# Kernel tuning notes

Measured on AMD Instinct MI355X. Metric: run time of the kernel, lower is better.

The kernel has to match this reference:

```python
import jax, jax.numpy as jnp
import numpy as np

N = 50000      # total nodes
C = 128        # in_channels
G = 4          # num_groups
B = 50         # number of graphs
NPG = N // B   # nodes per graph = 1000
E = 250000     # total edges (intra-graph)
COUT = 128     # conv out_channels


def setup_inputs() -> dict:
    key = jax.random.key(0)
    ks = jax.random.split(key, 6)
    sc = 1.0 / np.sqrt(C)
    x = jax.random.normal(ks[0], (N, C), dtype=jnp.float32)
    W_group = jax.random.normal(ks[1], (C, G), dtype=jnp.float32) * sc
    W_self = jax.random.normal(ks[2], (C, COUT), dtype=jnp.float32) * sc
    W_nbr = jax.random.normal(ks[3], (C, COUT), dtype=jnp.float32) * sc
    b = jnp.zeros((COUT,), dtype=jnp.float32)
    # intra-graph edges: E//B edges per graph, endpoints offset by graph id
    epg = E // B
    offs = (jnp.arange(E, dtype=jnp.int32) // epg) * NPG
    src = offs + jax.random.randint(ks[4], (E,), 0, NPG, dtype=jnp.int32)
    dst = offs + jax.random.randint(ks[5], (E,), 0, NPG, dtype=jnp.int32)
    edge_index = jnp.stack([src, dst])
    batch = (jnp.arange(N, dtype=jnp.int32) // NPG)
    # expanded node e = i*G*NPG + g*NPG + j maps back to original node i*NPG + j
    eidx = jnp.arange(G * N, dtype=jnp.int32)
    group_ptr = (eidx // (G * NPG)) * NPG + (eidx % NPG)
    return dict(x=x, W_group=W_group, W_self=W_self, W_nbr=W_nbr, b=b,
                edge_index=edge_index, batch=batch, group_ptr=group_ptr)


def reference(x, W_group, W_self, W_nbr, b, edge_index, batch, group_ptr):
    # soft group assignment: s = softmax(x @ W_group).T -> [G, N]
    s = jax.nn.softmax(x @ W_group, axis=-1).T
    # outer-product expansion: [G, N, C]
    ex = s[:, :, None] * x[None, :, :]
    # per-graph cat ordering: (g, graph i, local j) -> i*G*NPG + g*NPG + j
    ex = ex.reshape(G, B, NPG, C).transpose(1, 0, 2, 3).reshape(G * N, C)
    # expanded adjacency: replicate each graph's edges once per group
    src, dst = edge_index[0], edge_index[1]
    goff = jnp.arange(G, dtype=src.dtype)[:, None] * NPG            # [G, 1]
    src_exp = ((src // NPG) * (G * NPG))[None, :] + goff + (src % NPG)[None, :]
    dst_exp = ((dst // NPG) * (G * NPG))[None, :] + goff + (dst % NPG)[None, :]
    src_exp = src_exp.reshape(-1)
    dst_exp = dst_exp.reshape(-1)
    # GraphConv on expanded graph: self transform + sum-aggregated neighbor transform
    msg = (ex @ W_nbr)[src_exp]                                      # [G*E, COUT]
    agg = jax.ops.segment_sum(msg, dst_exp, num_segments=G * N)
    out = ex @ W_self + agg + b                                      # [G*N, COUT]
    # scatter-reduce G group copies back onto N original nodes
    return jax.ops.segment_sum(out, group_ptr, num_segments=N)
```

## Files before the change

### kernel.cpp

```cpp
#include <hip/hip_runtime.h>

constexpr int N_NODES  = 50000;
constexpr int C_IN     = 128;
constexpr int C_OUT    = 128;
constexpr int E_EDGES  = 250000;
constexpr int G_GRP    = 4;
constexpr int TM       = 32;
constexpr int CAP      = 32;
constexpr int NXCD     = 8;


typedef __attribute__((ext_vector_type(8))) short     short8;
typedef __attribute__((ext_vector_type(4))) float     f32x4;
typedef __attribute__((ext_vector_type(2))) unsigned  u32x2;

__device__ __forceinline__ unsigned short f2bf(float f) {
    unsigned u = __builtin_bit_cast(unsigned, f);
    u += 0x7fffu + ((u >> 16) & 1u);
    return (unsigned short)(u >> 16);
}
__device__ __forceinline__ unsigned pack2(float lo, float hi) {
    return (unsigned)f2bf(lo) | ((unsigned)f2bf(hi) << 16);
}

__device__ __forceinline__ int xcd_swizzle(int bid, int nblocks) {
    int q = nblocks / NXCD, r = nblocks % NXCD;
    int xcd = bid % NXCD, lid = bid / NXCD;
    return (xcd < r ? xcd * (q + 1) : r * (q + 1) + (xcd - r) * q) + lid;
}

constexpr int ZERO_BLOCKS  = (N_NODES / 4 + 255) / 256;
constexpr int WPREP_BLOCKS = (C_OUT * 256) / 256;

__global__ __launch_bounds__(256) void zero_prep_kernel(
    int* __restrict__ cnt,
    const float* __restrict__ Wself, const float* __restrict__ Wnbr,
    unsigned short* __restrict__ WT)
{
    int b = blockIdx.x;
    if (b < ZERO_BLOCKS) {
        int idx = b * 256 + threadIdx.x;
        if (idx < N_NODES / 4)
            reinterpret_cast<int4*>(cnt)[idx] = make_int4(0, 0, 0, 0);
    } else {
        int idx = (b - ZERO_BLOCKS) * 256 + threadIdx.x;
        int c = idx >> 8, k = idx & 255;
        float v = (k < 128) ? Wself[k * C_OUT + c] : Wnbr[(k - 128) * C_OUT + c];
        WT[idx] = f2bf(v);
    }
}

constexpr int EDGE_BLOCKS = (E_EDGES + 255) / 256;

__global__ __launch_bounds__(256) void fill_kernel(
    const int* __restrict__ src, const int* __restrict__ dst,
    int* __restrict__ cnt, int* __restrict__ buckets)
{
    int e = blockIdx.x * 256 + threadIdx.x;
    if (e < E_EDGES) {
        int d = dst[e];
        int pos = atomicAdd(&cnt[d], 1);
        if (pos < CAP) buckets[(size_t)d * CAP + pos] = src[e];
    }
}

constexpr int GATHER_BLOCKS = N_NODES / 8;

__global__ __launch_bounds__(256) void gather_kernel(
    const float* __restrict__ x,
    const int* __restrict__ cnt,
    const int* __restrict__ buckets,
    unsigned short* __restrict__ xa_bf)
{
    int wg   = xcd_swizzle(blockIdx.x, GATHER_BLOCKS);
    int tid  = threadIdx.x;
    int n    = wg * 8 + (tid >> 5);
    int q    = tid & 31;

    const float4* x4 = reinterpret_cast<const float4*>(x);
    int d = cnt[n];
    if (d > CAP) d = CAP;
    const int* sp = buckets + (size_t)n * CAP;

    float ax = 0.f, ay = 0.f, az = 0.f, aw = 0.f;
    int e = 0;
    for (; e + 4 <= d; e += 4) {
        int s0 = sp[e], s1 = sp[e + 1], s2 = sp[e + 2], s3 = sp[e + 3];
        float4 v0 = x4[(size_t)s0 * 32 + q];
        float4 v1 = x4[(size_t)s1 * 32 + q];
        float4 v2 = x4[(size_t)s2 * 32 + q];
        float4 v3 = x4[(size_t)s3 * 32 + q];
        ax += (v0.x + v1.x) + (v2.x + v3.x);
        ay += (v0.y + v1.y) + (v2.y + v3.y);
        az += (v0.z + v1.z) + (v2.z + v3.z);
        aw += (v0.w + v1.w) + (v2.w + v3.w);
    }
    for (; e < d; ++e) {
        int s = sp[e];
        float4 v = x4[(size_t)s * 32 + q];
        ax += v.x; ay += v.y; az += v.z; aw += v.w;
    }

    u32x2 pk{pack2(ax, ay), pack2(az, aw)};
    *reinterpret_cast<u32x2*>(&xa_bf[(size_t)n * 128 + q * 4]) = pk;
}

constexpr int GEMM_BLOCKS = (N_NODES + TM - 1) / TM;

__global__ __launch_bounds__(256) void mfma_gemm_kernel(
    const float* __restrict__ x,
    const unsigned short* __restrict__ xa_bf,
    const unsigned short* __restrict__ WT,
    const float* __restrict__ bias,
    float* __restrict__ out)
{
    __shared__ unsigned char Ab[TM * 512];

    int wg = xcd_swizzle(blockIdx.x, GEMM_BLOCKS);
    const int tid  = threadIdx.x;
    const int row0 = wg * TM;

    #pragma unroll
    for (int i = 0; i < 4; ++i) {
        int idx = tid + i * 256;
        int r = idx >> 5, q = idx & 31;
        int n = row0 + r;
        float4 v = make_float4(0.f, 0.f, 0.f, 0.f);
        if (n < N_NODES) v = reinterpret_cast<const float4*>(x)[(size_t)n * 32 + q];
        unsigned lo = pack2(v.x, v.y), hi = pack2(v.z, v.w);
        int byte = (r * 512 + q * 8) ^ ((r & 7) << 4);
        *reinterpret_cast<u32x2*>(&Ab[byte]) = u32x2{lo, hi};
    }

    #pragma unroll
    for (int i = 0; i < 4; ++i) {
        int idx = tid + i * 256;
        int r = idx >> 5, q = idx & 31;
        int n = row0 + r;
        u32x2 pk{0u, 0u};
        if (n < N_NODES)
            pk = *reinterpret_cast<const u32x2*>(&xa_bf[(size_t)n * 128 + q * 4]);
        int byte = (r * 512 + 256 + q * 8) ^ ((r & 7) << 4);
        *reinterpret_cast<u32x2*>(&Ab[byte]) = pk;
    }
    __syncthreads();

    const int lane = tid & 63;
    const int w    = tid >> 6;
    const int rt   = w >> 1;
    const int ct0  = (w & 1) * 4;

    short8 a[8];
    {
        int r  = rt * 16 + (lane & 15);
        int kb = (lane >> 4) * 16;
        #pragma unroll
        for (int ks = 0; ks < 8; ++ks) {
            int byte = (r * 512 + ks * 64 + kb) ^ ((r & 7) << 4);
            a[ks] = *reinterpret_cast<const short8*>(&Ab[byte]);
        }
    }

    #pragma unroll
    for (int cti = 0; cti < 4; ++cti) {
        int ct = ct0 + cti;
        int c  = ct * 16 + (lane & 15);
        const short8* bp = reinterpret_cast<const short8*>(WT + (size_t)c * 256)
                           + (lane >> 4);
        f32x4 acc = {0.f, 0.f, 0.f, 0.f};
        #pragma unroll
        for (int ks = 0; ks < 8; ++ks) {
            short8 b = bp[ks * 4];
            acc = __builtin_amdgcn_mfma_f32_16x16x32_bf16(a[ks], b, acc, 0, 0, 0);
        }
        float bv = (float)G_GRP * bias[c];
        #pragma unroll
        for (int i = 0; i < 4; ++i) {
            int rr = row0 + rt * 16 + (lane >> 4) * 4 + i;
            if (rr < N_NODES) out[(size_t)rr * C_OUT + c] = acc[i] + bv;
        }
    }
}

extern "C" void kernel_launch(void* const* d_in, const int* in_sizes, int n_in,
                              void* d_out, int out_size, void* d_ws, size_t ws_size,
                              hipStream_t stream)
{
    const float* x     = (const float*)d_in[0];
    const float* Wself = (const float*)d_in[2];
    const float* Wnbr  = (const float*)d_in[3];
    const float* bias  = (const float*)d_in[4];
    const int*   eidx  = (const int*)d_in[5];

    const int* src = eidx;
    const int* dst = eidx + E_EDGES;

    int* cnt     = (int*)d_ws;
    int* buckets = cnt + N_NODES;
    unsigned short* WT    = (unsigned short*)(buckets + (size_t)N_NODES * CAP);
    unsigned short* xa_bf = WT + (size_t)C_OUT * 256;

    float* out = (float*)d_out;

    zero_prep_kernel<<<ZERO_BLOCKS + WPREP_BLOCKS, 256, 0, stream>>>(
        cnt, Wself, Wnbr, WT);

    fill_kernel<<<EDGE_BLOCKS, 256, 0, stream>>>(src, dst, cnt, buckets);

    gather_kernel<<<GATHER_BLOCKS, 256, 0, stream>>>(x, cnt, buckets, xa_bf);

    mfma_gemm_kernel<<<GEMM_BLOCKS, 256, 0, stream>>>(
        x, xa_bf, WT, bias, out);
}
```

Before: 67.73 us.

## Fuse neighbor gather into MFMA GEMM kernel with branchless fixed-width bucket loads

Merges the gather and GEMM kernels into one 512-thread kernel that builds the aggregated neighbor rows straight into shared memory, dropping the xa_bf round trip through global memory and one launch. Buckets are pre-filled with each node's own index so the first 8 neighbor loads can be issued unconditionally and masked, which raises memory-level parallelism. The cost is zero-filling the whole 6.4MB bucket array every call, plus wasted loads for low-degree nodes and more register pressure.

```diff
diff --git a/kernel.cpp b/kernel.cpp
--- a/kernel.cpp
+++ b/kernel.cpp
@@ -5,9 +5,10 @@
 constexpr int C_OUT    = 128;
 constexpr int E_EDGES  = 250000;
 constexpr int G_GRP    = 4;
-constexpr int TM       = 32;
+constexpr int NXCD     = 8;
 constexpr int CAP      = 32;
-constexpr int NXCD     = 8;
+constexpr int CAP1     = 8;
+constexpr int TMF      = 64;
 
 
 typedef __attribute__((ext_vector_type(8))) short     short8;
@@ -22,28 +23,35 @@
 __device__ __forceinline__ unsigned pack2(float lo, float hi) {
     return (unsigned)f2bf(lo) | ((unsigned)f2bf(hi) << 16);
 }
-
 __device__ __forceinline__ int xcd_swizzle(int bid, int nblocks) {
     int q = nblocks / NXCD, r = nblocks % NXCD;
     int xcd = bid % NXCD, lid = bid / NXCD;
     return (xcd < r ? xcd * (q + 1) : r * (q + 1) + (xcd - r) * q) + lid;
 }
 
-constexpr int ZERO_BLOCKS  = (N_NODES / 4 + 255) / 256;
-constexpr int WPREP_BLOCKS = (C_OUT * 256) / 256;
+constexpr int BKT_I4   = N_NODES * CAP / 4;
+constexpr int BKT_BLKS = (BKT_I4 + 255) / 256;
+constexpr int CNT_BLKS = (N_NODES / 4 + 255) / 256;
+constexpr int WT_BLKS  = (C_OUT * 256) / 256;
 
 __global__ __launch_bounds__(256) void zero_prep_kernel(
-    int* __restrict__ cnt,
+    int* __restrict__ cnt, int* __restrict__ buckets,
     const float* __restrict__ Wself, const float* __restrict__ Wnbr,
     unsigned short* __restrict__ WT)
 {
     int b = blockIdx.x;
-    if (b < ZERO_BLOCKS) {
+    if (b < BKT_BLKS) {
         int idx = b * 256 + threadIdx.x;
+        if (idx < BKT_I4) {
+            int n = idx >> 3;
+            reinterpret_cast<int4*>(buckets)[idx] = make_int4(n, n, n, n);
+        }
+    } else if (b < BKT_BLKS + CNT_BLKS) {
+        int idx = (b - BKT_BLKS) * 256 + threadIdx.x;
         if (idx < N_NODES / 4)
             reinterpret_cast<int4*>(cnt)[idx] = make_int4(0, 0, 0, 0);
     } else {
-        int idx = (b - ZERO_BLOCKS) * 256 + threadIdx.x;
+        int idx = (b - BKT_BLKS - CNT_BLKS) * 256 + threadIdx.x;
         int c = idx >> 8, k = idx & 255;
         float v = (k < 128) ? Wself[k * C_OUT + c] : Wnbr[(k - 128) * C_OUT + c];
         WT[idx] = f2bf(v);
@@ -64,84 +72,72 @@
     }
 }
 
-constexpr int GATHER_BLOCKS = N_NODES / 8;
-
-__global__ __launch_bounds__(256) void gather_kernel(
+constexpr int FUSED_BLOCKS = (N_NODES + TMF - 1) / TMF;
+
+__global__ __launch_bounds__(512, 2) void fused_kernel(
     const float* __restrict__ x,
     const int* __restrict__ cnt,
     const int* __restrict__ buckets,
-    unsigned short* __restrict__ xa_bf)
-{
-    int wg   = xcd_swizzle(blockIdx.x, GATHER_BLOCKS);
-    int tid  = threadIdx.x;
-    int n    = wg * 8 + (tid >> 5);
-    int q    = tid & 31;
-
-    const float4* x4 = reinterpret_cast<const float4*>(x);
-    int d = cnt[n];
-    if (d > CAP) d = CAP;
-    const int* sp = buckets + (size_t)n * CAP;
-
-    float ax = 0.f, ay = 0.f, az = 0.f, aw = 0.f;
-    int e = 0;
-    for (; e + 4 <= d; e += 4) {
-        int s0 = sp[e], s1 = sp[e + 1], s2 = sp[e + 2], s3 = sp[e + 3];
-        float4 v0 = x4[(size_t)s0 * 32 + q];
-        float4 v1 = x4[(size_t)s1 * 32 + q];
-        float4 v2 = x4[(size_t)s2 * 32 + q];
-        float4 v3 = x4[(size_t)s3 * 32 + q];
-        ax += (v0.x + v1.x) + (v2.x + v3.x);
-        ay += (v0.y + v1.y) + (v2.y + v3.y);
-        az += (v0.z + v1.z) + (v2.z + v3.z);
-        aw += (v0.w + v1.w) + (v2.w + v3.w);
-    }
-    for (; e < d; ++e) {
-        int s = sp[e];
-        float4 v = x4[(size_t)s * 32 + q];
-        ax += v.x; ay += v.y; az += v.z; aw += v.w;
-    }
-
-    u32x2 pk{pack2(ax, ay), pack2(az, aw)};
-    *reinterpret_cast<u32x2*>(&xa_bf[(size_t)n * 128 + q * 4]) = pk;
-}
-
-constexpr int GEMM_BLOCKS = (N_NODES + TM - 1) / TM;
-
-__global__ __launch_bounds__(256) void mfma_gemm_kernel(
-    const float* __restrict__ x,
-    const unsigned short* __restrict__ xa_bf,
     const unsigned short* __restrict__ WT,
     const float* __restrict__ bias,
     float* __restrict__ out)
 {
-    __shared__ unsigned char Ab[TM * 512];
-
-    int wg = xcd_swizzle(blockIdx.x, GEMM_BLOCKS);
+    __shared__ unsigned char Ab[TMF * 512];
+
+    int wg = xcd_swizzle(blockIdx.x, FUSED_BLOCKS);
     const int tid  = threadIdx.x;
-    const int row0 = wg * TM;
+    const int row0 = wg * TMF;
 
     #pragma unroll
     for (int i = 0; i < 4; ++i) {
-        int idx = tid + i * 256;
+        int idx = tid + i * 512;
         int r = idx >> 5, q = idx & 31;
         int n = row0 + r;
         float4 v = make_float4(0.f, 0.f, 0.f, 0.f);
         if (n < N_NODES) v = reinterpret_cast<const float4*>(x)[(size_t)n * 32 + q];
-        unsigned lo = pack2(v.x, v.y), hi = pack2(v.z, v.w);
         int byte = (r * 512 + q * 8) ^ ((r & 7) << 4);
-        *reinterpret_cast<u32x2*>(&Ab[byte]) = u32x2{lo, hi};
-    }
-
-    #pragma unroll
-    for (int i = 0; i < 4; ++i) {
-        int idx = tid + i * 256;
-        int r = idx >> 5, q = idx & 31;
-        int n = row0 + r;
-        u32x2 pk{0u, 0u};
-        if (n < N_NODES)
-            pk = *reinterpret_cast<const u32x2*>(&xa_bf[(size_t)n * 128 + q * 4]);
-        int byte = (r * 512 + 256 + q * 8) ^ ((r & 7) << 4);
-        *reinterpret_cast<u32x2*>(&Ab[byte]) = pk;
+        *reinterpret_cast<u32x2*>(&Ab[byte]) = u32x2{pack2(v.x, v.y), pack2(v.z, v.w)};
+    }
+
+    {
+        const int slot = tid >> 5;
+        const int q    = tid & 31;
+        const float4* x4 = reinterpret_cast<const float4*>(x);
+        #pragma unroll
+        for (int h = 0; h < 4; ++h) {
+            int r  = slot + h * 16;
+            int n  = row0 + r;
+            int nc = (n < N_NODES) ? n : (N_NODES - 1);
+            int d  = cnt[nc];
+            if (d > CAP) d = CAP;
+            if (n >= N_NODES) d = 0;
+            const int4* sp4 = reinterpret_cast<const int4*>(buckets + (size_t)nc * CAP);
+
+            float ax = 0.f, ay = 0.f, az = 0.f, aw = 0.f;
+            {
+                int4 sA = sp4[0], sB = sp4[1];
+                int sl[8] = {sA.x, sA.y, sA.z, sA.w, sB.x, sB.y, sB.z, sB.w};
+                #pragma unroll
+                for (int k = 0; k < 8; ++k) {
+                    float4 v = x4[(size_t)sl[k] * 32 + q];
+                    if (k < d) { ax += v.x; ay += v.y; az += v.z; aw += v.w; }
+                }
+            }
+            if (d > CAP1) {
+                #pragma unroll
+                for (int t = 0; t < 3; ++t) {
+                    int4 sC = sp4[2 + 2 * t], sD = sp4[3 + 2 * t];
+                    int sl[8] = {sC.x, sC.y, sC.z, sC.w, sD.x, sD.y, sD.z, sD.w};
+                    #pragma unroll
+                    for (int k = 0; k < 8; ++k) {
+                        float4 v = x4[(size_t)sl[k] * 32 + q];
+                        if (8 + t * 8 + k < d) { ax += v.x; ay += v.y; az += v.z; aw += v.w; }
+                    }
+                }
+            }
+            int byte = (r * 512 + 256 + q * 8) ^ ((r & 7) << 4);
+            *reinterpret_cast<u32x2*>(&Ab[byte]) = u32x2{pack2(ax, ay), pack2(az, aw)};
+        }
     }
     __syncthreads();
 
@@ -163,21 +159,19 @@
 
     #pragma unroll
     for (int cti = 0; cti < 4; ++cti) {
-        int ct = ct0 + cti;
-        int c  = ct * 16 + (lane & 15);
+        int c = (ct0 + cti) * 16 + (lane & 15);
         const short8* bp = reinterpret_cast<const short8*>(WT + (size_t)c * 256)
                            + (lane >> 4);
         f32x4 acc = {0.f, 0.f, 0.f, 0.f};
         #pragma unroll
-        for (int ks = 0; ks < 8; ++ks) {
-            short8 b = bp[ks * 4];
-            acc = __builtin_amdgcn_mfma_f32_16x16x32_bf16(a[ks], b, acc, 0, 0, 0);
-        }
+        for (int ks = 0; ks < 8; ++ks)
+            acc = __builtin_amdgcn_mfma_f32_16x16x32_bf16(a[ks], bp[ks * 4],
+                                                          acc, 0, 0, 0);
         float bv = (float)G_GRP * bias[c];
         #pragma unroll
-        for (int i = 0; i < 4; ++i) {
-            int rr = row0 + rt * 16 + (lane >> 4) * 4 + i;
-            if (rr < N_NODES) out[(size_t)rr * C_OUT + c] = acc[i] + bv;
+        for (int ii = 0; ii < 4; ++ii) {
+            int rr = row0 + rt * 16 + (lane >> 4) * 4 + ii;
+            if (rr < N_NODES) out[(size_t)rr * C_OUT + c] = acc[ii] + bv;
         }
     }
 }
@@ -197,18 +191,14 @@
 
     int* cnt     = (int*)d_ws;
     int* buckets = cnt + N_NODES;
-    unsigned short* WT    = (unsigned short*)(buckets + (size_t)N_NODES * CAP);
-    unsigned short* xa_bf = WT + (size_t)C_OUT * 256;
+    unsigned short* WT = (unsigned short*)(buckets + (size_t)N_NODES * CAP);
 
     float* out = (float*)d_out;
 
-    zero_prep_kernel<<<ZERO_BLOCKS + WPREP_BLOCKS, 256, 0, stream>>>(
-        cnt, Wself, Wnbr, WT);
+    zero_prep_kernel<<<BKT_BLKS + CNT_BLKS + WT_BLKS, 256, 0, stream>>>(
+        cnt, buckets, Wself, Wnbr, WT);
 
     fill_kernel<<<EDGE_BLOCKS, 256, 0, stream>>>(src, dst, cnt, buckets);
 
-    gather_kernel<<<GATHER_BLOCKS, 256, 0, stream>>>(x, cnt, buckets, xa_bf);
-
-    mfma_gemm_kernel<<<GEMM_BLOCKS, 256, 0, stream>>>(
-        x, xa_bf, WT, bias, out);
-}
+    fused_kernel<<<FUSED_BLOCKS, 512, 0, stream>>>(x, cnt, buckets, WT, bias, out);
+}
```

Result: slower. 70.25 us (+3.7%).
